# Performance work log

Hardware: AMD Instinct MI355X
Metric: run time of the kernel (lower is better)

Reference implementation:

```python
import jax, jax.numpy as jnp
import numpy as np
import math

N_HEADS = 12
ROPE_DIM = 64
BASE = 10000.0


def _rope_tables(seq_len, dim):
    inv_freq = 1.0 / (BASE ** (jnp.arange(0, dim, 2, dtype=jnp.float32) / dim))
    t = jnp.arange(seq_len, dtype=jnp.float32)
    freqs = jnp.outer(t, inv_freq)                      # [S, dim/2]
    emb = jnp.concatenate([freqs, freqs], axis=-1)      # [S, dim]
    # broadcast shape [1, S, 1, dim]
    return jnp.cos(emb)[None, :, None, :], jnp.sin(emb)[None, :, None, :]


def _rotate_half(x):
    x1, x2 = jnp.split(x, 2, axis=-1)
    return jnp.concatenate([-x2, x1], axis=-1)


def setup_inputs() -> dict:
    key = jax.random.key(0)
    ks = jax.random.split(key, 9)
    B, S, E = 2, 2048, 768
    s = 1.0 / math.sqrt(E)
    return {
        "x": jax.random.normal(ks[0], (B, S, E), jnp.float32),
        "Wq": jax.random.normal(ks[1], (E, E), jnp.float32) * s,
        "bq": jax.random.normal(ks[2], (E,), jnp.float32) * 0.02,
        "Wk": jax.random.normal(ks[3], (E, E), jnp.float32) * s,
        "bk": jax.random.normal(ks[4], (E,), jnp.float32) * 0.02,
        "Wv": jax.random.normal(ks[5], (E, E), jnp.float32) * s,
        "bv": jax.random.normal(ks[6], (E,), jnp.float32) * 0.02,
        "Wp": jax.random.normal(ks[7], (E, E), jnp.float32) * s,
        "bp": jax.random.normal(ks[8], (E,), jnp.float32) * 0.02,
    }


def reference(x, Wq, bq, Wk, bk, Wv, bv, Wp, bp):
    B, S, E = x.shape
    H = N_HEADS
    D = E // H

    q = (x @ Wq + bq).reshape(B, S, H, D)
    k = (x @ Wk + bk).reshape(B, S, H, D)
    v = (x @ Wv + bv).reshape(B, S, H, D)

    # rotary on first ROPE_DIM dims (here ROPE_DIM == D, so full rotary)
    cos, sin = _rope_tables(S, ROPE_DIM)
    q_rot, q_pass = q[..., :ROPE_DIM], q[..., ROPE_DIM:]
    k_rot, k_pass = k[..., :ROPE_DIM], k[..., ROPE_DIM:]
    q_rot = q_rot * cos + _rotate_half(q_rot) * sin
    k_rot = k_rot * cos + _rotate_half(k_rot) * sin
    q = jnp.concatenate([q_rot, q_pass], axis=-1)
    k = jnp.concatenate([k_rot, k_pass], axis=-1)

    # scores [B, M, N, H]; mask before scaling (as in the torch code; -inf unchanged)
    att = jnp.einsum("bmhd,bnhd->bmnh", q, k)
    causal = jnp.tril(jnp.ones((S, S), dtype=bool))[None, :, :, None]
    att = jnp.where(causal, att, -jnp.inf)
    att = jax.nn.softmax(att / math.sqrt(D), axis=2)
    out = jnp.einsum("bmnh,bnhd->bmhd", att, v)

    return out.reshape(B, S, E) @ Wp + bp
```

## Files before the change

### kernel.cpp

```cpp
#include <hip/hip_runtime.h>
#include <stdint.h>

#define S_LEN 2048
#define EMB   768
#define NH    12
#define DH    64
#define M_TOT 4096
#define WELEM 589824
#define QELEM 3145728

typedef float  floatx4  __attribute__((ext_vector_type(4)));
typedef float  floatx16 __attribute__((ext_vector_type(16)));
typedef __bf16 bf16x8  __attribute__((ext_vector_type(8)));
typedef __bf16 bf16x4  __attribute__((ext_vector_type(4)));
typedef unsigned short ushortx4 __attribute__((ext_vector_type(4)));

__device__ __forceinline__ unsigned short f2bf(float f) {
    union { float f; unsigned u; } v; v.f = f;
    unsigned u = v.u;
    unsigned r = (u + 0x7FFFu + ((u >> 16) & 1u)) >> 16;
    return (unsigned short)r;
}

__device__ __forceinline__ void gl_lds16(const void* g, void* l) {
    __builtin_amdgcn_global_load_lds(
        (__attribute__((address_space(1))) const void*)g,
        (__attribute__((address_space(3))) void*)l, 16, 0, 0);
}

__global__ void cvt_all_kernel(const float* __restrict__ x, unsigned short* __restrict__ xb,
                               const float* __restrict__ W0, const float* __restrict__ W1,
                               const float* __restrict__ W2, const float* __restrict__ W3,
                               unsigned short* __restrict__ WT_all, float2* __restrict__ rope) {
    __shared__ float t[64][65];
    const int blk = blockIdx.x;
    if (blk < 3072) {
        int i = (blk * 256 + threadIdx.x) * 4;
        float4 v = *(const float4*)(x + i);
        ushortx4 r = { f2bf(v.x), f2bf(v.y), f2bf(v.z), f2bf(v.w) };
        *(ushortx4*)(xb + i) = r;
        return;
    }
    if (blk >= 3648) {
        int idx = (blk - 3648) * 256 + threadIdx.x;
        int s = idx >> 5, d = idx & 31;
        float f = exp2f((float)d * -0.41524101186092034f);
        float th = (float)s * f;
        float sn, cs; sincosf(th, &sn, &cs);
        rope[idx] = make_float2(cs, sn);
        return;
    }
    const int tc = blk - 3072;
    const int z = tc / 144, rr0 = tc % 144;
    const float* W = (z == 0) ? W0 : (z == 1 ? W1 : (z == 2 ? W2 : W3));
    unsigned short* O = WT_all + (size_t)z * WELEM;
    const int k0 = (rr0 % 12) * 64, n0 = (rr0 / 12) * 64;
    const int c = threadIdx.x & 63, r4 = threadIdx.x >> 6;
#pragma unroll
    for (int rr = 0; rr < 64; rr += 4) {
        int r = rr + r4;
        t[r][c] = W[(size_t)(k0 + r) * EMB + n0 + c];
    }
    __syncthreads();
#pragma unroll
    for (int rr = 0; rr < 64; rr += 4) {
        int nn = rr + r4;
        O[(size_t)(n0 + nn) * EMB + k0 + c] = f2bf(t[c][nn]);
    }
}

template<int BM, int BN, int WM, int WN>
static __device__ __forceinline__ void gemm_core(
    const unsigned short* __restrict__ A, const unsigned short* __restrict__ BT,
    int m0, int n0, int K, int tid, floatx4 (&acc)[WM / 16][WN / 16],
    unsigned short* Als, unsigned short* Bls)
{
    const int lane = tid & 63;
    const int c0 = lane & 15, quad = lane >> 4;
    const int wave = tid >> 6;
    const int NWN = BN / WN;
    const int wm = (wave / NWN) * WM, wn = (wave % NWN) * WN;

    for (int k0 = 0; k0 < K; k0 += 64) {
        __syncthreads();
#pragma unroll
        for (int it = 0; it < BM / 32; ++it) {
            int ch = it * 256 + tid;
            int row = ch >> 3, sc = ch & 7;
            int cc = sc ^ (row & 7);
            gl_lds16(A + (size_t)(m0 + row) * K + k0 + cc * 8, Als + ch * 8);
        }
#pragma unroll
        for (int it = 0; it < BN / 32; ++it) {
            int ch = it * 256 + tid;
            int row = ch >> 3, sc = ch & 7;
            int cc = sc ^ (row & 7);
            gl_lds16(BT + (size_t)(n0 + row) * K + k0 + cc * 8, Bls + ch * 8);
        }
        __syncthreads();
        bf16x8 af[WM / 16][2], bfv[WN / 16][2];
#pragma unroll
        for (int ii = 0; ii < WM / 16; ++ii) {
            int row = wm + 16 * ii + c0;
#pragma unroll
            for (int h = 0; h < 2; ++h)
                af[ii][h] = *(const bf16x8*)(Als + row * 64 + (((4 * h + quad) ^ (row & 7)) * 8));
        }
#pragma unroll
        for (int jj = 0; jj < WN / 16; ++jj) {
            int row = wn + 16 * jj + c0;
#pragma unroll
            for (int h = 0; h < 2; ++h)
                bfv[jj][h] = *(const bf16x8*)(Bls + row * 64 + (((4 * h + quad) ^ (row & 7)) * 8));
        }
#pragma unroll
        for (int ii = 0; ii < WM / 16; ++ii)
#pragma unroll
            for (int jj = 0; jj < WN / 16; ++jj) {
                acc[ii][jj] = __builtin_amdgcn_mfma_f32_16x16x32_bf16(af[ii][0], bfv[jj][0], acc[ii][jj], 0, 0, 0);
                acc[ii][jj] = __builtin_amdgcn_mfma_f32_16x16x32_bf16(af[ii][1], bfv[jj][1], acc[ii][jj], 0, 0, 0);
            }
    }
}

__global__ __launch_bounds__(256, 4) void qkv_kernel(
    const unsigned short* __restrict__ xb, const unsigned short* __restrict__ WT_all,
    const float* __restrict__ bq, const float* __restrict__ bk, const float* __restrict__ bv,
    const float2* __restrict__ rope, unsigned short* __restrict__ qkv_out)
{
    __shared__ __align__(16) unsigned short Als[64 * 64];
    __shared__ __align__(16) unsigned short Bls[128 * 64];
    const int z = blockIdx.z;
    const float* bias = (z == 0) ? bq : (z == 1 ? bk : bv);
    __bf16* Cout = (__bf16*)(qkv_out + (size_t)z * QELEM);
    const int m0 = blockIdx.x * 64, n0 = blockIdx.y * 128;
    const int tid = threadIdx.x, lane = tid & 63, c0 = lane & 15, quad = lane >> 4, wave = tid >> 6;
    const int wm = (wave >> 1) * 32, wn = (wave & 1) * 64;

    floatx4 acc[2][4] = {};
    gemm_core<64, 128, 32, 64>(xb, WT_all + (size_t)z * WELEM, m0, n0, EMB, tid, acc, Als, Bls);

    if (z == 2) {
#pragma unroll
        for (int ii = 0; ii < 2; ++ii) {
            int m = m0 + wm + 16 * ii + quad * 4;
            int b = m >> 11, s = m & (S_LEN - 1);
#pragma unroll
            for (int jj = 0; jj < 4; ++jj) {
                int n = n0 + wn + 16 * jj + c0;
                int h = n >> 6, d = n & 63;
                float bn = bias[n];
                bf16x4 pv;
#pragma unroll
                for (int r = 0; r < 4; ++r) pv[r] = (__bf16)(acc[ii][jj][r] + bn);
                *(bf16x4*)(Cout + ((size_t)(b * NH + h) * DH + d) * S_LEN + s) = pv;
            }
        }
        return;
    }

#pragma unroll
    for (int ii = 0; ii < 2; ++ii) {
#pragma unroll
        for (int r = 0; r < 4; ++r) {
            int m = m0 + wm + 16 * ii + quad * 4 + r;
            int b = m >> 11, s = m & (S_LEN - 1);
            float vals[4];
#pragma unroll
            for (int jj = 0; jj < 4; ++jj) vals[jj] = acc[ii][jj][r] + bias[n0 + wn + 16 * jj + c0];
#pragma unroll
            for (int jj = 0; jj < 2; ++jj) {
                int d = 16 * jj + c0;
                float2 t = rope[s * 32 + d];
                float lo = vals[jj], hi = vals[jj + 2];
                vals[jj]     = lo * t.x - hi * t.y;
                vals[jj + 2] = hi * t.x + lo * t.y;
            }
            if (z == 0) {
#pragma unroll
                for (int jj = 0; jj < 4; ++jj) vals[jj] *= 0.18033688011112042f;
            }
#pragma unroll
            for (int jj = 0; jj < 4; ++jj) {
                int n = n0 + wn + 16 * jj + c0;
                int h = n >> 6, d = n & 63;
                Cout[((size_t)(b * NH + h) * S_LEN + s) * DH + d] = (__bf16)vals[jj];
            }
        }
    }
}

__global__ __launch_bounds__(256, 3) void flash_kernel(
    const unsigned short* __restrict__ Qg, const unsigned short* __restrict__ Kg,
    const unsigned short* __restrict__ Vt, unsigned short* __restrict__ Og)
{
    __shared__ __align__(16) unsigned short Kls[3][64 * 64];
    __shared__ __align__(16) unsigned short Vls[3][64 * 64];
    __shared__ float lred[2][64];

    const int i = blockIdx.x;
    const int kk = i >> 8, g = i & 255;
    const int r0 = (kk == 0) ? g : (kk == 1 ? 511 - g : 512 + g);
    const int qt = 31 - r0 / 24;
    const int bh = r0 % 24;
    const int b = bh / NH, h = bh % NH;
    const int m0 = qt * 64;
    const int tid = threadIdx.x, lane = tid & 63, wave = tid >> 6;
    const int wm2 = wave >> 1, wn2 = wave & 1;
    const int lr = lane & 31, hf = lane >> 5;
    const size_t base = (size_t)bh * S_LEN * DH;
    const int mrow = m0 + wm2 * 32 + lr;

    bf16x8 qf[4];
#pragma unroll
    for (int t = 0; t < 4; ++t)
        qf[t] = *(const bf16x8*)(Qg + base + (size_t)mrow * DH + 16 * t + 8 * hf);
    asm volatile("" :: "v"(qf[0]), "v"(qf[1]), "v"(qf[2]), "v"(qf[3]));

    floatx16 oa0 = {}, oa1 = {};
    float l_lane = 0.f;
    const float C = 23.083120654223414f;
    const int ntiles = qt + 1;

#define STAGE_TILE(T, BUF)                                                              \
    {                                                                                   \
        _Pragma("unroll")                                                               \
        for (int it = 0; it < 2; ++it) {                                                \
            int ch = it * 256 + tid;                                                    \
            int row = ch >> 3, cc = (ch & 7) ^ (row & 7);                               \
            gl_lds16(Kg + base + (size_t)((T) * 64 + row) * DH + cc * 8,                \
                     &Kls[BUF][ch * 8]);                                                \
            gl_lds16(Vt + base + (size_t)row * S_LEN + (T) * 64 + cc * 8,               \
                     &Vls[BUF][ch * 8]);                                                \
        }                                                                               \
    }

    STAGE_TILE(0, 0);
    if (ntiles > 1) STAGE_TILE(1, 1);

    for (int nt = 0; nt < ntiles; ++nt) {
        const int buf = nt % 3;
        if (nt + 1 < ntiles) asm volatile("s_waitcnt vmcnt(4)" ::: "memory");
        else                 asm volatile("s_waitcnt vmcnt(0)" ::: "memory");
        __builtin_amdgcn_s_barrier();
        asm volatile("" ::: "memory");
        if (nt + 2 < ntiles) STAGE_TILE(nt + 2, (nt + 2) % 3);
        const unsigned short* Kb = Kls[buf];
        const unsigned short* Vb = Vls[buf];

        floatx16 sa = {};
        __builtin_amdgcn_s_setprio(1);
#pragma unroll
        for (int t = 0; t < 4; ++t) {
            int row = wn2 * 32 + lr;
            int ck = (2 * t + hf) ^ (row & 7);
            bf16x8 kf = *(const bf16x8*)(Kb + row * 64 + ck * 8);
            sa = __builtin_amdgcn_mfma_f32_32x32x16_bf16(kf, qf[t], sa, 0, 0, 0);
        }
        __builtin_amdgcn_s_setprio(0);

        if (nt == ntiles - 1) {
#pragma unroll
            for (int r = 0; r < 16; ++r) {
                int n = nt * 64 + wn2 * 32 + (r & 3) + 8 * (r >> 2) + 4 * hf;
                if (n > mrow) sa[r] = -1e30f;
            }
        }

        unsigned W[8];
#pragma unroll
        for (int q = 0; q < 8; ++q) {
            float p0 = __builtin_amdgcn_exp2f(sa[2 * q] - C);
            float p1 = __builtin_amdgcn_exp2f(sa[2 * q + 1] - C);
            l_lane += p0 + p1;
            union { __bf16 bb[2]; unsigned u; } w;
            w.bb[0] = (__bf16)p0; w.bb[1] = (__bf16)p1;
            W[q] = w.u;
        }
        bf16x8 pb[2];
#pragma unroll
        for (int t2 = 0; t2 < 2; ++t2) {
            unsigned own0 = hf ? W[4 * t2 + 2] : W[4 * t2 + 0];
            unsigned own1 = hf ? W[4 * t2 + 3] : W[4 * t2 + 1];
            unsigned giv0 = hf ? W[4 * t2 + 0] : W[4 * t2 + 2];
            unsigned giv1 = hf ? W[4 * t2 + 1] : W[4 * t2 + 3];
            unsigned s0 = (unsigned)__shfl_xor((int)giv0, 32, 64);
            unsigned s1 = (unsigned)__shfl_xor((int)giv1, 32, 64);
            union { unsigned u[4]; bf16x8 v; } pk;
            pk.u[0] = hf ? s0 : own0;
            pk.u[1] = hf ? s1 : own1;
            pk.u[2] = hf ? own0 : s0;
            pk.u[3] = hf ? own1 : s1;
            pb[t2] = pk.v;
        }

        __builtin_amdgcn_s_setprio(1);
#pragma unroll
        for (int dt = 0; dt < 2; ++dt) {
            int d = 32 * dt + lr;
#pragma unroll
            for (int t2 = 0; t2 < 2; ++t2) {
                int cv = (wn2 * 4 + 2 * t2 + hf) ^ (d & 7);
                bf16x8 vf = *(const bf16x8*)(Vb + d * 64 + cv * 8);
                if (dt == 0) oa0 = __builtin_amdgcn_mfma_f32_32x32x16_bf16(vf, pb[t2], oa0, 0, 0, 0);
                else         oa1 = __builtin_amdgcn_mfma_f32_32x32x16_bf16(vf, pb[t2], oa1, 0, 0, 0);
            }
        }
        __builtin_amdgcn_s_setprio(0);
    }
#undef STAGE_TILE

    l_lane += __shfl_xor(l_lane, 32, 64);

    __syncthreads();
    float* red = (float*)&Kls[0][0];
    if (wn2 == 1) {
#pragma unroll
        for (int e = 0; e < 16; ++e) red[(wm2 * 32 + e) * 64 + lane]        = oa0[e];
#pragma unroll
        for (int e = 0; e < 16; ++e) red[(wm2 * 32 + 16 + e) * 64 + lane]   = oa1[e];
        lred[wm2][lane] = l_lane;
    }
    __syncthreads();
    if (wn2 == 0) {
        const float lt = l_lane + lred[wm2][lane];
        const float rl = 1.0f / lt;
        __bf16* Ob16 = (__bf16*)Og;
#pragma unroll
        for (int rg = 0; rg < 4; ++rg) {
            bf16x4 ov0, ov1;
#pragma unroll
            for (int j = 0; j < 4; ++j) {
                int e = rg * 4 + j;
                ov0[j] = (__bf16)((oa0[e] + red[(wm2 * 32 + e) * 64 + lane]) * rl);
                ov1[j] = (__bf16)((oa1[e] + red[(wm2 * 32 + 16 + e) * 64 + lane]) * rl);
            }
            int d = 8 * rg + 4 * hf;
            *(bf16x4*)(Ob16 + ((size_t)(b * S_LEN + mrow)) * EMB + h * DH + d)      = ov0;
            *(bf16x4*)(Ob16 + ((size_t)(b * S_LEN + mrow)) * EMB + h * DH + 32 + d) = ov1;
        }
    }
}

__global__ __launch_bounds__(256, 4) void proj_kernel(
    const unsigned short* __restrict__ Ob, const unsigned short* __restrict__ WpT,
    const float* __restrict__ bp, float* __restrict__ out)
{
    __shared__ __align__(16) unsigned short Als[64 * 64];
    __shared__ __align__(16) unsigned short Bls[64 * 64];
    const int m0 = blockIdx.x * 64, n0 = blockIdx.y * 64;
    const int tid = threadIdx.x, lane = tid & 63, c0 = lane & 15, quad = lane >> 4, wave = tid >> 6;
    const int wm = (wave >> 1) * 32, wn = (wave & 1) * 32;

    floatx4 acc[2][2] = {};
    gemm_core<64, 64, 32, 32>(Ob, WpT, m0, n0, EMB, tid, acc, Als, Bls);

#pragma unroll
    for (int ii = 0; ii < 2; ++ii)
#pragma unroll
        for (int r = 0; r < 4; ++r) {
            int m = m0 + wm + 16 * ii + quad * 4 + r;
#pragma unroll
            for (int jj = 0; jj < 2; ++jj) {
                int n = n0 + wn + 16 * jj + c0;
                out[(size_t)m * EMB + n] = acc[ii][jj][r] + bp[n];
            }
        }
}

extern "C" void kernel_launch(void* const* d_in, const int* in_sizes, int n_in,
                              void* d_out, int out_size, void* d_ws, size_t ws_size,
                              hipStream_t stream)
{
    (void)in_sizes; (void)n_in; (void)out_size;
    const float* x  = (const float*)d_in[0];
    const float* Wq = (const float*)d_in[1];
    const float* bq = (const float*)d_in[2];
    const float* Wk = (const float*)d_in[3];
    const float* bk = (const float*)d_in[4];
    const float* Wv = (const float*)d_in[5];
    const float* bv = (const float*)d_in[6];
    const float* Wp = (const float*)d_in[7];
    const float* bp = (const float*)d_in[8];

    unsigned short* ws  = (unsigned short*)d_ws;
    unsigned short* xb  = ws;
    unsigned short* WT  = xb + (size_t)QELEM;
    unsigned short* QKV = WT + 4 * (size_t)WELEM;
    unsigned short* Ob  = QKV + 3 * (size_t)QELEM;
    float2* rope = (float2*)(Ob + (size_t)QELEM);
    if (ws_size < ((size_t)QELEM * 5 + 4 * (size_t)WELEM) * 2 + 2048 * 32 * 8) return;

    cvt_all_kernel<<<3904, 256, 0, stream>>>(x, xb, Wq, Wk, Wv, Wp, WT, rope);
    qkv_kernel<<<dim3(64, 6, 3), 256, 0, stream>>>(xb, WT, bq, bk, bv, (const float2*)rope, QKV);
    flash_kernel<<<dim3(768), 256, 0, stream>>>(QKV, QKV + QELEM, QKV + 2 * (size_t)QELEM, Ob);
    proj_kernel<<<dim3(64, 12), 256, 0, stream>>>(Ob, WT + 3 * (size_t)WELEM, bp, (float*)d_out);
}
```

Before: 151.9 us.

## Fuse Q, K, V projections into one block per head sharing the x tile

The QKV kernel now gives each block a 64-row by 64-column head slice and computes the Q, K and V outputs together. One x tile in LDS is reused across all three weight matrices, replacing the separate z-grid launch that reloaded x for each projection. The grid drops from 1152 to 768 blocks, and each block uses more LDS and more accumulator registers (launch bounds lowered to 3). The rope and V-transpose epilogues are rewritten to match the new per-head tile mapping. The inline k-loop appears to replace the shared gemm_core helper and has no double buffering.

```diff
diff --git a/kernel.cpp b/kernel.cpp
--- a/kernel.cpp
+++ b/kernel.cpp
@@ -123,69 +123,101 @@
     }
 }
 
-__global__ __launch_bounds__(256, 4) void qkv_kernel(
+__global__ __launch_bounds__(256, 3) void qkv_kernel(
     const unsigned short* __restrict__ xb, const unsigned short* __restrict__ WT_all,
     const float* __restrict__ bq, const float* __restrict__ bk, const float* __restrict__ bv,
     const float2* __restrict__ rope, unsigned short* __restrict__ qkv_out)
 {
     __shared__ __align__(16) unsigned short Als[64 * 64];
-    __shared__ __align__(16) unsigned short Bls[128 * 64];
-    const int z = blockIdx.z;
-    const float* bias = (z == 0) ? bq : (z == 1 ? bk : bv);
-    __bf16* Cout = (__bf16*)(qkv_out + (size_t)z * QELEM);
-    const int m0 = blockIdx.x * 64, n0 = blockIdx.y * 128;
+    __shared__ __align__(16) unsigned short Bls[3][64 * 64];
+    const int m0 = blockIdx.x * 64, n0 = blockIdx.y * 64;
     const int tid = threadIdx.x, lane = tid & 63, c0 = lane & 15, quad = lane >> 4, wave = tid >> 6;
-    const int wm = (wave >> 1) * 32, wn = (wave & 1) * 64;
-
-    floatx4 acc[2][4] = {};
-    gemm_core<64, 128, 32, 64>(xb, WT_all + (size_t)z * WELEM, m0, n0, EMB, tid, acc, Als, Bls);
-
-    if (z == 2) {
+    const int wm = (wave >> 1) * 32, wn2 = wave & 1;
+    const int h = n0 >> 6;
+
+    floatx4 acc[3][2][2] = {};
+
+    for (int k0 = 0; k0 < EMB; k0 += 64) {
+        __syncthreads();
+#pragma unroll
+        for (int it = 0; it < 2; ++it) {
+            int ch = it * 256 + tid;
+            int row = ch >> 3, cc = (ch & 7) ^ (row & 7);
+            gl_lds16(xb + (size_t)(m0 + row) * EMB + k0 + cc * 8, Als + ch * 8);
+        }
+#pragma unroll
+        for (int z = 0; z < 3; ++z)
+#pragma unroll
+            for (int it = 0; it < 2; ++it) {
+                int ch = it * 256 + tid;
+                int row = ch >> 3, cc = (ch & 7) ^ (row & 7);
+                gl_lds16(WT_all + (size_t)z * WELEM + (size_t)(n0 + row) * EMB + k0 + cc * 8,
+                         &Bls[z][ch * 8]);
+            }
+        __syncthreads();
+        bf16x8 af[2][2];
+#pragma unroll
+        for (int ii = 0; ii < 2; ++ii) {
+            int row = wm + 16 * ii + c0;
+#pragma unroll
+            for (int hh = 0; hh < 2; ++hh)
+                af[ii][hh] = *(const bf16x8*)(Als + row * 64 + (((4 * hh + quad) ^ (row & 7)) * 8));
+        }
+#pragma unroll
+        for (int z = 0; z < 3; ++z) {
+#pragma unroll
+            for (int jj = 0; jj < 2; ++jj) {
+                int row = 16 * wn2 + 32 * jj + c0;
+                bf16x8 b0 = *(const bf16x8*)(&Bls[z][row * 64 + ((quad ^ (row & 7)) * 8)]);
+                bf16x8 b1 = *(const bf16x8*)(&Bls[z][row * 64 + (((4 + quad) ^ (row & 7)) * 8)]);
+#pragma unroll
+                for (int ii = 0; ii < 2; ++ii) {
+                    acc[z][ii][jj] = __builtin_amdgcn_mfma_f32_16x16x32_bf16(af[ii][0], b0, acc[z][ii][jj], 0, 0, 0);
+                    acc[z][ii][jj] = __builtin_amdgcn_mfma_f32_16x16x32_bf16(af[ii][1], b1, acc[z][ii][jj], 0, 0, 0);
+                }
+            }
+        }
+    }
+
+    const int dlo = 16 * wn2 + c0;
+#pragma unroll
+    for (int z = 0; z < 2; ++z) {
+        const float* bias = z ? bk : bq;
+        __bf16* Cout = (__bf16*)(qkv_out + (size_t)z * QELEM);
+        float b0 = bias[n0 + dlo], b1 = bias[n0 + dlo + 32];
+#pragma unroll
+        for (int ii = 0; ii < 2; ++ii) {
+#pragma unroll
+            for (int r = 0; r < 4; ++r) {
+                int m = m0 + wm + 16 * ii + quad * 4 + r;
+                int b = m >> 11, s = m & (S_LEN - 1);
+                float lo = acc[z][ii][0][r] + b0;
+                float hi = acc[z][ii][1][r] + b1;
+                float2 t = rope[s * 32 + dlo];
+                float v0 = lo * t.x - hi * t.y;
+                float v1 = hi * t.x + lo * t.y;
+                if (z == 0) { v0 *= 0.18033688011112042f; v1 *= 0.18033688011112042f; }
+                __bf16* row = Cout + ((size_t)(b * NH + h) * S_LEN + s) * DH;
+                row[dlo]      = (__bf16)v0;
+                row[dlo + 32] = (__bf16)v1;
+            }
+        }
+    }
+    {
+        __bf16* Cout = (__bf16*)(qkv_out + (size_t)2 * QELEM);
+        float b0 = bv[n0 + dlo], b1 = bv[n0 + dlo + 32];
 #pragma unroll
         for (int ii = 0; ii < 2; ++ii) {
             int m = m0 + wm + 16 * ii + quad * 4;
             int b = m >> 11, s = m & (S_LEN - 1);
-#pragma unroll
-            for (int jj = 0; jj < 4; ++jj) {
-                int n = n0 + wn + 16 * jj + c0;
-                int h = n >> 6, d = n & 63;
-                float bn = bias[n];
-                bf16x4 pv;
-#pragma unroll
-                for (int r = 0; r < 4; ++r) pv[r] = (__bf16)(acc[ii][jj][r] + bn);
-                *(bf16x4*)(Cout + ((size_t)(b * NH + h) * DH + d) * S_LEN + s) = pv;
-            }
-        }
-        return;
-    }
-
-#pragma unroll
-    for (int ii = 0; ii < 2; ++ii) {
-#pragma unroll
-        for (int r = 0; r < 4; ++r) {
-            int m = m0 + wm + 16 * ii + quad * 4 + r;
-            int b = m >> 11, s = m & (S_LEN - 1);
-            float vals[4];
-#pragma unroll
-            for (int jj = 0; jj < 4; ++jj) vals[jj] = acc[ii][jj][r] + bias[n0 + wn + 16 * jj + c0];
-#pragma unroll
-            for (int jj = 0; jj < 2; ++jj) {
-                int d = 16 * jj + c0;
-                float2 t = rope[s * 32 + d];
-                float lo = vals[jj], hi = vals[jj + 2];
-                vals[jj]     = lo * t.x - hi * t.y;
-                vals[jj + 2] = hi * t.x + lo * t.y;
-            }
-            if (z == 0) {
-#pragma unroll
-                for (int jj = 0; jj < 4; ++jj) vals[jj] *= 0.18033688011112042f;
-            }
-#pragma unroll
-            for (int jj = 0; jj < 4; ++jj) {
-                int n = n0 + wn + 16 * jj + c0;
-                int h = n >> 6, d = n & 63;
-                Cout[((size_t)(b * NH + h) * S_LEN + s) * DH + d] = (__bf16)vals[jj];
-            }
+            bf16x4 p0, p1;
+#pragma unroll
+            for (int r = 0; r < 4; ++r) {
+                p0[r] = (__bf16)(acc[2][ii][0][r] + b0);
+                p1[r] = (__bf16)(acc[2][ii][1][r] + b1);
+            }
+            *(bf16x4*)(Cout + ((size_t)(b * NH + h) * DH + dlo)      * S_LEN + s) = p0;
+            *(bf16x4*)(Cout + ((size_t)(b * NH + h) * DH + dlo + 32) * S_LEN + s) = p1;
         }
     }
 }
@@ -392,7 +424,7 @@
     if (ws_size < ((size_t)QELEM * 5 + 4 * (size_t)WELEM) * 2 + 2048 * 32 * 8) return;
 
     cvt_all_kernel<<<3904, 256, 0, stream>>>(x, xb, Wq, Wk, Wv, Wp, WT, rope);
-    qkv_kernel<<<dim3(64, 6, 3), 256, 0, stream>>>(xb, WT, bq, bk, bv, (const float2*)rope, QKV);
+    qkv_kernel<<<dim3(64, 12), 256, 0, stream>>>(xb, WT, bq, bk, bv, (const float2*)rope, QKV);
     flash_kernel<<<dim3(768), 256, 0, stream>>>(QKV, QKV + QELEM, QKV + 2 * (size_t)QELEM, Ob);
     proj_kernel<<<dim3(64, 12), 256, 0, stream>>>(Ob, WT + 3 * (size_t)WELEM, bp, (float*)d_out);
 }
```

New measurement: 149.7 us. Within noise of the previous version (-1.4%).
